# Kernel optimization log

Hardware: AMD Instinct MI355X
Metric: run time of the kernel (lower is better)

## Reference

```python
import jax, jax.numpy as jnp
import numpy as np

B, T, C, U = 16, 128, 64, 128
ODE_UNFOLDS = 6
EPS = 1e-8


def setup_inputs() -> dict:
    key = jax.random.key(0)
    ks = jax.random.split(key, 12)
    u = lambda k, s, lo, hi: jax.random.uniform(k, s, jnp.float32, lo, hi)
    return dict(
        x=jax.random.normal(ks[0], (B, T, C), jnp.float32),
        h0=jnp.zeros((B, U), jnp.float32),
        gleak=u(ks[1], (U,), 0.001, 1.0),
        vleak=u(ks[2], (U,), -0.2, 0.2),
        cm=u(ks[3], (U,), 0.4, 0.6),
        sigma=u(ks[4], (U, U), 3.0, 8.0),
        mu=u(ks[5], (U, U), 0.3, 0.8),
        w=u(ks[6], (U, U), 0.001, 1.0),
        erev=jnp.sign(jax.random.normal(ks[7], (U, U))).astype(jnp.float32),
        sensory_sigma=u(ks[8], (C, U), 3.0, 8.0),
        sensory_mu=u(ks[9], (C, U), 0.3, 0.8),
        sensory_w=u(ks[10], (C, U), 0.001, 1.0),
        sensory_erev=jnp.sign(jax.random.normal(ks[11], (C, U))).astype(jnp.float32),
        input_w=jnp.ones((C,), jnp.float32),
        input_b=jnp.zeros((C,), jnp.float32),
        output_w=jnp.ones((U,), jnp.float32),
        output_b=jnp.zeros((U,), jnp.float32),
    )


def reference(x, h0, gleak, vleak, cm, sigma, mu, w, erev,
              sensory_sigma, sensory_mu, sensory_w, sensory_erev,
              input_w, input_b, output_w, output_b):
    sp = jax.nn.softplus
    # Positive-constrained params (implicit_param_constraints=True)
    w_pos = sp(w)                      # [U,U]
    sw_pos = sp(sensory_w)             # [C,U]
    gl = sp(gleak)                     # [U]
    # elapsed_time ts = 1.0 -> cm_t = softplus(cm) / (1/ode_unfolds)
    cm_t = sp(cm) * ODE_UNFOLDS        # [U]

    def step(h, xt):
        # input affine mapping
        xt = xt * input_w + input_b                                        # [B,C]
        # sensory synapses (constant across unfolds)
        sens_act = sw_pos * jax.nn.sigmoid(sensory_sigma * (xt[:, :, None] - sensory_mu))  # [B,C,U]
        w_num_s = jnp.sum(sens_act * sensory_erev, axis=1)                 # [B,U]
        w_den_s = jnp.sum(sens_act, axis=1)                                # [B,U]
        v = h
        for _ in range(ODE_UNFOLDS):
            # recurrent synapses: pre dim 1, post dim 2
            w_act = w_pos * jax.nn.sigmoid(sigma * (v[:, :, None] - mu))   # [B,U,U]
            w_num = jnp.sum(w_act * erev, axis=1) + w_num_s                # [B,U]
            w_den = jnp.sum(w_act, axis=1) + w_den_s                       # [B,U]
            num = cm_t * v + gl * vleak + w_num
            den = cm_t + gl + w_den
            v = num / (den + EPS)
        out = v * output_w + output_b   # motor_size == units for FullyConnected
        return v, out

    h_final, outs = jax.lax.scan(step, h0, jnp.swapaxes(x, 0, 1))  # outs: [T,B,U]
    readout = jnp.swapaxes(outs, 0, 1)                             # [B,T,U]
    return readout, h_final
```

## Files before the change

### kernel.cpp

```cpp
#include <hip/hip_runtime.h>

#define NB 16
#define NT 128
#define NC 64
#define NU 128
#define UNFOLDS 6
#define LTC_EPS 1e-8f
#define LOG2E 1.44269504088896340736f
#define LN2   0.69314718055994530942f

__device__ __forceinline__ float fast_softplus(float x) {
    return LN2 * __builtin_amdgcn_logf(1.0f + __builtin_amdgcn_exp2f(x * LOG2E));
}

template<int CTRL>
__device__ __forceinline__ float qperm(float x) {
    return __int_as_float(__builtin_amdgcn_update_dpp(
        0, __float_as_int(x), CTRL, 0xF, 0xF, true));
}
__device__ __forceinline__ float quad_sum(float x) {
    x += qperm<0xB1>(x);
    x += qperm<0x4E>(x);
    return x;
}

__global__ __launch_bounds__(128)
void ltc_sens_kernel(const float* __restrict__ x,
                     const float* __restrict__ ssigma,
                     const float* __restrict__ smu,
                     const float* __restrict__ sw,
                     const float* __restrict__ serev,
                     const float* __restrict__ iw,
                     const float* __restrict__ ib,
                     float2* __restrict__ sens)
{
    __shared__ float xt[NC];
    const int blk = blockIdx.x;
    const int b = blk >> 7;
    const int t = blk & (NT - 1);
    const int j = threadIdx.x;
    if (j < NC) xt[j] = fmaf(x[(b * NT + t) * NC + j], iw[j], ib[j]);
    __syncthreads();

    float n0 = 0.f, n1 = 0.f, d0 = 0.f, d1 = 0.f;
#pragma unroll 8
    for (int c = 0; c < NC; ++c) {
        const int idx = c * NU + j;
        float sg = ssigma[idx];
        float m  = smu[idx];
        float wp = fast_softplus(sw[idx]);
        float er = serev[idx];
        float tt = (m - xt[c]) * (sg * LOG2E);
        float e  = __builtin_amdgcn_exp2f(tt);
        float r  = __builtin_amdgcn_rcpf(1.0f + e);
        float wr = wp * r;
        if (c & 1) { n1 = fmaf(wr, er, n1); d1 += wr; }
        else       { n0 = fmaf(wr, er, n0); d0 += wr; }
    }
    sens[(b * NT + t) * NU + j] = make_float2(n0 + n1, d0 + d1);
}

__global__ __launch_bounds__(512, 2)
void ltc_seq_kernel(const float* __restrict__ h0,
                    const float* __restrict__ gleak,
                    const float* __restrict__ vleak,
                    const float* __restrict__ cm,
                    const float* __restrict__ sigma,
                    const float* __restrict__ mu,
                    const float* __restrict__ w,
                    const float* __restrict__ erev,
                    const float* __restrict__ ow,
                    const float* __restrict__ ob,
                    const float2* __restrict__ sens,
                    float* __restrict__ out)
{
    __shared__ __align__(16) float v_lds[2][NU];

    const int tid = threadIdx.x;
    const int b   = blockIdx.x;
    const int j   = tid >> 2;
    const int k   = tid & 3;

    float rA[32], rB[32], rW[32];
#pragma unroll
    for (int q = 0; q < 8; ++q) {
        const int g = (q + 2 * k) & 7;
#pragma unroll
        for (int i = 0; i < 4; ++i) {
            const int c   = q * 4 + i;
            const int idx = ((k << 5) + (g << 2) + i) * NU + j;
            float sg = sigma[idx];
            float m  = mu[idx];
            float wp = fast_softplus(w[idx]);
            float er = erev[idx];
            float a  = -sg * LOG2E;
            rA[c] = a;
            rB[c] = -a * m;
            rW[c] = wp * er;
        }
    }
#pragma unroll
    for (int c = 0; c < 32; ++c) {
        asm volatile("" : "+v"(rA[c]));
        asm volatile("" : "+v"(rB[c]));
        asm volatile("" : "+v"(rW[c]));
    }

    const float cmt = 6.0f * fast_softplus(cm[j]);
    const float gl  = fast_softplus(gleak[j]);
    const float glv = gl * vleak[j];
    const float owj = ow[j];
    const float obj = ob[j];
    float vj = h0[b * NU + j];
    if (k == 0) v_lds[0][j] = vj;
    __syncthreads();

    int p = 0;
    float2 s_cur = sens[b * NT * NU + j];

    for (int t = 0; t < NT; ++t) {
        const float snum = s_cur.x;
        const float sden = s_cur.y;
        const int tn = (t + 1 < NT) ? (t + 1) : t;
        const float2 s_next = sens[(b * NT + tn) * NU + j];

#pragma unroll
        for (int u = 0; u < UNFOLDS; ++u) {
            float4 vvq[8];
#pragma unroll
            for (int q = 0; q < 8; ++q) {
                const int g = (q + 2 * k) & 7;
                vvq[q] = *(const float4*)&v_lds[p][(k << 5) + (g << 2)];
            }
            float n0 = 0.f, n1 = 0.f, d0 = 0.f, d1 = 0.f;
#pragma unroll
            for (int q = 0; q < 8; ++q) {
                const float vv[4] = { vvq[q].x, vvq[q].y, vvq[q].z, vvq[q].w };
#pragma unroll
                for (int i = 0; i < 4; ++i) {
                    const int c = q * 4 + i;
                    float tt = fmaf(rA[c], vv[i], rB[c]);
                    float e  = __builtin_amdgcn_exp2f(tt);
                    float r  = __builtin_amdgcn_rcpf(1.0f + e);
                    if (i & 1) { n1 = fmaf(rW[c], r, n1); d1 = fmaf(fabsf(rW[c]), r, d1); }
                    else       { n0 = fmaf(rW[c], r, n0); d0 = fmaf(fabsf(rW[c]), r, d0); }
                }
            }
            const float wn = quad_sum(n0 + n1) + snum;
            const float wd = quad_sum(d0 + d1) + sden;
            const float numf = fmaf(cmt, vj, glv) + wn;
            const float denf = cmt + gl + wd + LTC_EPS;
            vj = numf * __builtin_amdgcn_rcpf(denf);
            if (k == 0) v_lds[p ^ 1][j] = vj;
            __syncthreads();
            p ^= 1;
        }

        if (k == 0) out[(b * NT + t) * NU + j] = fmaf(vj, owj, obj);
        s_cur = s_next;
    }
    if (k == 0) out[NB * NT * NU + b * NU + j] = vj;
}

extern "C" void kernel_launch(void* const* d_in, const int* in_sizes, int n_in,
                              void* d_out, int out_size, void* d_ws, size_t ws_size,
                              hipStream_t stream) {
    const float* x      = (const float*)d_in[0];
    const float* h0     = (const float*)d_in[1];
    const float* gleak  = (const float*)d_in[2];
    const float* vleak  = (const float*)d_in[3];
    const float* cm     = (const float*)d_in[4];
    const float* sigma  = (const float*)d_in[5];
    const float* mu     = (const float*)d_in[6];
    const float* w      = (const float*)d_in[7];
    const float* erev   = (const float*)d_in[8];
    const float* ssig   = (const float*)d_in[9];
    const float* smu    = (const float*)d_in[10];
    const float* sw     = (const float*)d_in[11];
    const float* serev  = (const float*)d_in[12];
    const float* iw     = (const float*)d_in[13];
    const float* ibv    = (const float*)d_in[14];
    const float* ow     = (const float*)d_in[15];
    const float* ob     = (const float*)d_in[16];
    float* out = (float*)d_out;

    float2* sens = (float2*)d_ws;
    ltc_sens_kernel<<<NB * NT, 128, 0, stream>>>(x, ssig, smu, sw, serev, iw, ibv, sens);
    ltc_seq_kernel<<<NB, 512, 0, stream>>>(h0, gleak, vleak, cm, sigma, mu, w, erev,
                                           ow, ob, (const float2*)sens, out);
}
```

Measured before the change: 824.5 us.

## Split recurrent reduction across eight lanes per unit with packed float2 math

The sequential kernel now uses 1024 threads per batch block, so each output unit's 128-element presynaptic sum is split across 8 lanes of 16 elements instead of 4 lanes of 32. The final reduction gains a ds_swizzle step. Arithmetic is written on 2-wide float vectors to encourage packed FMA, and |w| is precomputed. This shortens the per-unfold serial latency of the critical recurrence, at the cost of larger barriers and an extra cross-lane step.

Result: faster. 764.6 us (-7.3%).

```diff
diff --git a/kernel.cpp b/kernel.cpp
--- a/kernel.cpp
+++ b/kernel.cpp
@@ -9,6 +9,8 @@
 #define LOG2E 1.44269504088896340736f
 #define LN2   0.69314718055994530942f
 
+typedef float f32x2 __attribute__((ext_vector_type(2)));
+
 __device__ __forceinline__ float fast_softplus(float x) {
     return LN2 * __builtin_amdgcn_logf(1.0f + __builtin_amdgcn_exp2f(x * LOG2E));
 }
@@ -18,9 +20,10 @@
     return __int_as_float(__builtin_amdgcn_update_dpp(
         0, __float_as_int(x), CTRL, 0xF, 0xF, true));
 }
-__device__ __forceinline__ float quad_sum(float x) {
+__device__ __forceinline__ float sum8(float x) {
     x += qperm<0xB1>(x);
     x += qperm<0x4E>(x);
+    x += __int_as_float(__builtin_amdgcn_ds_swizzle(__float_as_int(x), 0x101F));
     return x;
 }
 
@@ -60,7 +63,7 @@
     sens[(b * NT + t) * NU + j] = make_float2(n0 + n1, d0 + d1);
 }
 
-__global__ __launch_bounds__(512, 2)
+__global__ __launch_bounds__(1024, 4)
 void ltc_seq_kernel(const float* __restrict__ h0,
                     const float* __restrict__ gleak,
                     const float* __restrict__ vleak,
@@ -78,39 +81,40 @@
 
     const int tid = threadIdx.x;
     const int b   = blockIdx.x;
-    const int j   = tid >> 2;
-    const int k   = tid & 3;
+    const int j   = tid >> 3;
+    const int k   = tid & 7;
 
-    float rA[32], rB[32], rW[32];
+    f32x2 rA2[8], rB2[8], rW2[8], aW2[8];
 #pragma unroll
     for (int q = 0; q < 8; ++q) {
-        const int g = (q + 2 * k) & 7;
-#pragma unroll
-        for (int i = 0; i < 4; ++i) {
-            const int c   = q * 4 + i;
-            const int idx = ((k << 5) + (g << 2) + i) * NU + j;
-            float sg = sigma[idx];
-            float m  = mu[idx];
-            float wp = fast_softplus(w[idx]);
-            float er = erev[idx];
-            float a  = -sg * LOG2E;
-            rA[c] = a;
-            rB[c] = -a * m;
-            rW[c] = wp * er;
-        }
+        const int g   = (q + k) & 7;
+        const int i0  = (k << 4) + (g << 1);
+        const int id0 = i0 * NU + j;
+        const int id1 = id0 + NU;
+        const float sg0 = sigma[id0], sg1 = sigma[id1];
+        const float m0  = mu[id0],    m1  = mu[id1];
+        const float wp0 = fast_softplus(w[id0]), wp1 = fast_softplus(w[id1]);
+        const float er0 = erev[id0],  er1 = erev[id1];
+        f32x2 a;  a.x = -sg0 * LOG2E;  a.y = -sg1 * LOG2E;
+        f32x2 bb; bb.x = -a.x * m0;    bb.y = -a.y * m1;
+        f32x2 ww; ww.x = wp0 * er0;    ww.y = wp1 * er1;
+        f32x2 aw; aw.x = wp0;          aw.y = wp1;
+        rA2[q] = a; rB2[q] = bb; rW2[q] = ww; aW2[q] = aw;
     }
 #pragma unroll
-    for (int c = 0; c < 32; ++c) {
-        asm volatile("" : "+v"(rA[c]));
-        asm volatile("" : "+v"(rB[c]));
-        asm volatile("" : "+v"(rW[c]));
+    for (int q = 0; q < 8; ++q) {
+        asm volatile("" : "+v"(rA2[q]));
+        asm volatile("" : "+v"(rB2[q]));
+        asm volatile("" : "+v"(rW2[q]));
+        asm volatile("" : "+v"(aW2[q]));
     }
 
-    const float cmt = 6.0f * fast_softplus(cm[j]);
-    const float gl  = fast_softplus(gleak[j]);
-    const float glv = gl * vleak[j];
-    const float owj = ow[j];
-    const float obj = ob[j];
+    const float cmt    = 6.0f * fast_softplus(cm[j]);
+    const float gl     = fast_softplus(gleak[j]);
+    const float glv    = gl * vleak[j];
+    const float cmt_gl = cmt + gl + LTC_EPS;
+    const float owj    = ow[j];
+    const float obj    = ob[j];
     float vj = h0[b * NU + j];
     if (k == 0) v_lds[0][j] = vj;
     __syncthreads();
@@ -126,30 +130,27 @@
 
 #pragma unroll
         for (int u = 0; u < UNFOLDS; ++u) {
-            float4 vvq[8];
+            f32x2 n2 = {0.f, 0.f};
+            f32x2 d2 = {0.f, 0.f};
 #pragma unroll
             for (int q = 0; q < 8; ++q) {
-                const int g = (q + 2 * k) & 7;
-                vvq[q] = *(const float4*)&v_lds[p][(k << 5) + (g << 2)];
+                const int g = (q + k) & 7;
+                const f32x2 v2 = *(const f32x2*)&v_lds[p][(k << 4) + (g << 1)];
+                f32x2 t2 = rA2[q] * v2 + rB2[q];
+                f32x2 e2;
+                e2.x = __builtin_amdgcn_exp2f(t2.x);
+                e2.y = __builtin_amdgcn_exp2f(t2.y);
+                f32x2 u2 = e2 + (f32x2){1.0f, 1.0f};
+                f32x2 r2;
+                r2.x = __builtin_amdgcn_rcpf(u2.x);
+                r2.y = __builtin_amdgcn_rcpf(u2.y);
+                n2 = rW2[q] * r2 + n2;
+                d2 = aW2[q] * r2 + d2;
             }
-            float n0 = 0.f, n1 = 0.f, d0 = 0.f, d1 = 0.f;
-#pragma unroll
-            for (int q = 0; q < 8; ++q) {
-                const float vv[4] = { vvq[q].x, vvq[q].y, vvq[q].z, vvq[q].w };
-#pragma unroll
-                for (int i = 0; i < 4; ++i) {
-                    const int c = q * 4 + i;
-                    float tt = fmaf(rA[c], vv[i], rB[c]);
-                    float e  = __builtin_amdgcn_exp2f(tt);
-                    float r  = __builtin_amdgcn_rcpf(1.0f + e);
-                    if (i & 1) { n1 = fmaf(rW[c], r, n1); d1 = fmaf(fabsf(rW[c]), r, d1); }
-                    else       { n0 = fmaf(rW[c], r, n0); d0 = fmaf(fabsf(rW[c]), r, d0); }
-                }
-            }
-            const float wn = quad_sum(n0 + n1) + snum;
-            const float wd = quad_sum(d0 + d1) + sden;
+            const float wn = sum8(n2.x + n2.y) + snum;
+            const float wd = sum8(d2.x + d2.y) + sden;
             const float numf = fmaf(cmt, vj, glv) + wn;
-            const float denf = cmt + gl + wd + LTC_EPS;
+            const float denf = cmt_gl + wd;
             vj = numf * __builtin_amdgcn_rcpf(denf);
             if (k == 0) v_lds[p ^ 1][j] = vj;
             __syncthreads();
@@ -186,6 +187,6 @@
 
     float2* sens = (float2*)d_ws;
     ltc_sens_kernel<<<NB * NT, 128, 0, stream>>>(x, ssig, smu, sw, serev, iw, ibv, sens);
-    ltc_seq_kernel<<<NB, 512, 0, stream>>>(h0, gleak, vleak, cm, sigma, mu, w, erev,
-                                           ow, ob, (const float2*)sens, out);
+    ltc_seq_kernel<<<NB, 1024, 0, stream>>>(h0, gleak, vleak, cm, sigma, mu, w, erev,
+                                            ow, ob, (const float2*)sens, out);
 }
```
